# Kernel optimization log

Hardware: AMD Instinct MI355X
Metric: run time of the kernel (lower is better)

## Reference

```python
import jax, jax.numpy as jnp
import numpy as np

V, D, DFF, E, K, L = 32000, 1024, 4096, 8, 2, 2
B, S = 2, 1024


def _layer_norm(x, scale, bias, eps=1e-5):
    mu = jnp.mean(x, axis=-1, keepdims=True)
    var = jnp.var(x, axis=-1, keepdims=True)
    return (x - mu) * jax.lax.rsqrt(var + eps) * scale + bias


def setup_inputs() -> dict:
    key = jax.random.key(0)
    ks = jax.random.split(key, 16)
    s = 0.02
    return {
        "input_ids": jax.random.randint(ks[0], (B, S), 0, V, dtype=jnp.int32),
        "emb": jax.random.normal(ks[1], (V, D), jnp.float32) * s,
        "t_ln_scale": jnp.ones((L, D), jnp.float32),
        "t_ln_bias": jnp.zeros((L, D), jnp.float32),
        "t_w1": jax.random.normal(ks[2], (L, D, DFF), jnp.float32) * s,
        "t_b1": jnp.zeros((L, DFF), jnp.float32),
        "t_w2": jax.random.normal(ks[3], (L, DFF, D), jnp.float32) * s,
        "t_b2": jnp.zeros((L, D), jnp.float32),
        "Wr": jax.random.normal(ks[4], (D, E), jnp.float32) * s,
        "br": jnp.zeros((E,), jnp.float32),
        "e_w1": jax.random.normal(ks[5], (E, D, DFF), jnp.float32) * s,
        "e_b1": jnp.zeros((E, DFF), jnp.float32),
        "e_w2": jax.random.normal(ks[6], (E, DFF, D), jnp.float32) * s,
        "e_b2": jnp.zeros((E, D), jnp.float32),
        "Wl": jax.random.normal(ks[7], (D, V), jnp.float32) * s,
        "bl": jnp.zeros((V,), jnp.float32),
    }


def reference(input_ids, emb, t_ln_scale, t_ln_bias, t_w1, t_b1, t_w2, t_b2,
              Wr, br, e_w1, e_b1, e_w2, e_b2, Wl, bl):
    # token embeddings: [B,S,D]
    x = emb[input_ids]

    # temporal abstraction: L pre-LN residual MLP blocks
    for l in range(L):
        h = _layer_norm(x, t_ln_scale[l], t_ln_bias[l])
        h = jax.nn.gelu(jnp.einsum('bsd,df->bsf', h, t_w1[l]) + t_b1[l])
        x = x + jnp.einsum('bsf,fd->bsd', h, t_w2[l]) + t_b2[l]

    # router: top-k renormalized softmax over experts, scattered to [B,S,E]
    r_logits = jnp.einsum('bsd,de->bse', x, Wr) + br
    top_vals, top_idx = jax.lax.top_k(r_logits, K)
    top_w = jax.nn.softmax(top_vals, axis=-1)
    routing_weights = jnp.put_along_axis(
        jnp.zeros_like(r_logits), top_idx, top_w, axis=-1, inplace=False)

    # dense all-experts stack: [B,S,E,D]
    h = jax.nn.gelu(jnp.einsum('bsd,edf->bsef', x, e_w1) + e_b1)
    expert_out = jnp.einsum('bsef,efd->bsed', h, e_w2) + e_b2

    # sparse-weighted combine
    y = jnp.einsum('bse,bsed->bsd', routing_weights, expert_out)

    logits = jnp.einsum('bsd,dv->bsv', y, Wl) + bl
    return logits, routing_weights
```

## Files before the change

kernel.cpp:

```cpp
#include <hip/hip_runtime.h>
#include <stdint.h>

typedef __bf16 bf16;
typedef __bf16 bf16x8 __attribute__((ext_vector_type(8)));
typedef float f32x4 __attribute__((ext_vector_type(4)));

#define DEV __device__ __forceinline__

static constexpr int Dm   = 1024;
static constexpr int DFFm = 4096;
static constexpr int Tm   = 2048;
static constexpr int Vm   = 32000;

#define GLOAD_LDS16(g, l)                                                      \
  __builtin_amdgcn_global_load_lds(                                            \
      (const __attribute__((address_space(1))) unsigned int*)(g),              \
      (__attribute__((address_space(3))) unsigned int*)(l), 16, 0, 0)

DEV float gelu_tanh(float v) {
  float u = 0.7978845608028654f * (v + 0.044715f * v * v * v);
  float e = __expf(2.0f * u);
  float t = 1.0f - 2.0f / (e + 1.0f);
  return 0.5f * v * (1.0f + t);
}

enum { EPI_GELU_SPLIT = 0, EPI_RESID = 1, EPI_GELU_BF16 = 2, EPI_MOE = 3, EPI_BIAS = 4 };

struct GemmP {
  const bf16* Ah;
  const bf16* Bh;
  const float* bias;
  const float* rwp;
  const int* cnt;
  const int* idx;
  float* outF;
  bf16* outH;
  int K; int N;
  int lda; int ldb; int ldo;
  long aBS, bBS, outBS;
  int biasBS;
  int ebase;
  int kcShift; int kcK;
};

template <int EPI, bool GATHER, bool SWZ>
__launch_bounds__(256, 2)
__global__ void gemm_bt(GemmP p) {
  __shared__ bf16 lds[16384];
  bf16* ldsA = lds;
  bf16* ldsB = lds + 8192;

  const int tid  = threadIdx.x;
  const int lane = tid & 63;
  const int wid  = tid >> 6;
  const int wr   = wid >> 1;
  const int wc   = wid & 1;
  const int z    = blockIdx.z;
  const int kc   = z & ((1 << p.kcShift) - 1);
  const int ze   = z >> p.kcShift;

  int bx = blockIdx.x, by = blockIdx.y;
  if constexpr (SWZ) {
    const int gx = gridDim.x, gy = gridDim.y;
    const int nwg = gx * gy;
    const int lin = by * gx + bx;
    const int q = nwg >> 3, r = nwg & 7;
    const int xcd = lin & 7, loc = lin >> 3;
    const int nid = (xcd < r ? xcd * (q + 1) : r * (q + 1) + (xcd - r) * q) + loc;
    bx = nid / gy; by = nid % gy;
  }

  const long am0 = (long)by * 128;
  const long bn0 = (long)bx * 128;

  int cntE = 0;
  const int* il = nullptr;
  if constexpr (GATHER || EPI == EPI_MOE) {
    cntE = p.cnt[p.ebase + ze];
    if (am0 >= cntE) return;
    il = p.idx + (long)(p.ebase + ze) * 2048;
  }

  const long lda = p.lda, ldb = p.ldb;
  const long K = p.K;
  const long kco = (long)kc * p.kcK;

  const int sub = (lane & 7) ^ (lane >> 3);
  const int rIn = wid * 8 + (lane >> 3);

  const bf16 *aS[4], *bS[4];
  {
    const bf16* Bb = p.Bh + (long)ze * p.bBS + kco + bn0 * ldb;
    const bf16* Ab = p.Ah + (long)ze * p.aBS + kco + am0 * lda;
#pragma unroll
    for (int j = 0; j < 4; ++j) {
      const int row = j * 32 + rIn;
      bS[j] = Bb + (long)row * ldb + sub * 8;
      if constexpr (GATHER) {
        const int rt = (int)am0 + row;
        const long grow = il[rt < cntE ? rt : 0];
        aS[j] = p.Ah + grow * lda + kco + sub * 8;
      } else {
        aS[j] = Ab + (long)row * lda + sub * 8;
      }
    }
  }
  char* dstA[4];
#pragma unroll
  for (int j = 0; j < 4; ++j)
    dstA[j] = (char*)(void*)lds + (j * 256 + wid * 64) * 16;

  f32x4 acc[4][4] = {};

  const int r15 = lane & 15;
  const int kcs = lane >> 4;
  const int xk  = lane & 7;

  for (long k0 = 0; k0 < K; k0 += 64) {
    __syncthreads();
#pragma unroll
    for (int j = 0; j < 4; ++j) {
      GLOAD_LDS16(aS[j] + k0, dstA[j]);
      GLOAD_LDS16(bS[j] + k0, dstA[j] + 16384);
    }
    __syncthreads();
#pragma unroll
    for (int h = 0; h < 2; ++h) {
      const int q8 = ((kcs + 4 * h) ^ xk) << 3;
      bf16x8 a[4], b[4];
#pragma unroll
      for (int m = 0; m < 4; ++m)
        a[m] = *(const bf16x8*)(ldsA + (wr * 64 + m * 16 + r15) * 64 + q8);
#pragma unroll
      for (int n = 0; n < 4; ++n)
        b[n] = *(const bf16x8*)(ldsB + (wc * 64 + n * 16 + r15) * 64 + q8);
#pragma unroll
      for (int m = 0; m < 4; ++m)
#pragma unroll
        for (int n = 0; n < 4; ++n)
          acc[m][n] = __builtin_amdgcn_mfma_f32_16x16x32_bf16(a[m], b[n], acc[m][n], 0, 0, 0);
    }
  }

  const long N = p.N;

#pragma unroll
  for (int m = 0; m < 4; ++m) {
#pragma unroll
    for (int n = 0; n < 4; ++n) {
      const long col = bn0 + wc * 64 + n * 16 + (lane & 15);
      const float bv = (kc == 0) ? p.bias[(long)ze * p.biasBS + col] : 0.0f;
#pragma unroll
      for (int r = 0; r < 4; ++r) {
        const long row = am0 + wr * 64 + m * 16 + (lane >> 4) * 4 + r;
        float v = acc[m][n][r] + bv;
        if constexpr (EPI == EPI_GELU_SPLIT) {
          float g = gelu_tanh(v);
          bf16 hh = (bf16)g;
          long o = row * (long)p.ldo + col;
          p.outH[o] = hh;
          p.outH[o + N] = (bf16)(g - (float)hh);
          p.outH[o + 2 * N] = hh;
        } else if constexpr (EPI == EPI_RESID) {
          atomicAdd(p.outF + row * N + col, v);
        } else if constexpr (EPI == EPI_GELU_BF16) {
          long o = (long)ze * p.outBS + row * N + col;
          p.outH[o] = (bf16)gelu_tanh(v);
        } else if constexpr (EPI == EPI_MOE) {
          if (row < cntE) {
            const int tok = il[row];
            const float wgt = p.rwp[(long)tok * 8 + p.ebase + ze];
            atomicAdd(p.outF + (long)tok * N + col, wgt * v);
          }
        } else {
          p.outF[row * N + col] = v;
        }
      }
    }
  }
}

template <bool AUG>
__global__ void transpose_cvt(const float* __restrict__ in, bf16* __restrict__ out,
                              int R, int C, long inBS, long outBS) {
  __shared__ float tile[32][33];
  const float* inp = in + (long)blockIdx.z * inBS;
  const long c0 = (long)blockIdx.x * 32;
  const long r0 = (long)blockIdx.y * 32;
  const int tx = threadIdx.x;
  const int ty = threadIdx.y;
#pragma unroll
  for (int i = 0; i < 4; ++i) {
    int r = ty + i * 8;
    tile[r][tx] = inp[(r0 + r) * (long)C + c0 + tx];
  }
  __syncthreads();
  const long ob = (long)blockIdx.z * outBS;
  const long stride = AUG ? 3L * R : (long)R;
#pragma unroll
  for (int i = 0; i < 4; ++i) {
    int c = ty + i * 8;
    float v = tile[tx][c];
    bf16 h = (bf16)v;
    long o = ob + (c0 + c) * stride + r0 + tx;
    out[o] = h;
    if constexpr (AUG) {
      out[o + R] = h;
      out[o + 2 * R] = (bf16)(v - (float)h);
    }
  }
}

__global__ void embed_kernel(const int* __restrict__ ids, const float* __restrict__ emb,
                             float* __restrict__ x) {
  const long t = blockIdx.x;
  const int id = ids[t];
  ((float4*)(x + t * 1024))[threadIdx.x] = ((const float4*)(emb + (long)id * 1024))[threadIdx.x];
}

__global__ void ln_aug_kernel(const float* __restrict__ x, const float* __restrict__ sc,
                              const float* __restrict__ bi, bf16* __restrict__ oa) {
  const long t = blockIdx.x;
  const int tid = threadIdx.x;
  const int lane = tid & 63, wid = tid >> 6;
  float4 a = ((const float4*)(x + t * 1024))[tid];
  float s = a.x + a.y + a.z + a.w;
  float q = a.x * a.x + a.y * a.y + a.z * a.z + a.w * a.w;
#pragma unroll
  for (int off = 32; off; off >>= 1) {
    s += __shfl_down(s, off);
    q += __shfl_down(q, off);
  }
  __shared__ float sr[4], qr[4];
  if (lane == 0) { sr[wid] = s; qr[wid] = q; }
  __syncthreads();
  s = sr[0] + sr[1] + sr[2] + sr[3];
  q = qr[0] + qr[1] + qr[2] + qr[3];
  const float mu = s * (1.0f / 1024.0f);
  const float var = q * (1.0f / 1024.0f) - mu * mu;
  const float rs = rsqrtf(var + 1e-5f);
#pragma unroll
  for (int j = 0; j < 4; ++j) {
    const int d = tid * 4 + j;
    const float g = (((const float*)&a)[j] - mu) * rs * sc[d] + bi[d];
    const bf16 h = (bf16)g;
    oa[t * 3072 + d] = h;
    oa[t * 3072 + 1024 + d] = (bf16)(g - (float)h);
    oa[t * 3072 + 2048 + d] = h;
  }
}

__global__ void router_kernel(const float* __restrict__ x, const float* __restrict__ Wr,
                              const float* __restrict__ br, float* __restrict__ rwo,
                              int* __restrict__ top2) {
  const long t = blockIdx.x;
  const int lane = threadIdx.x;
  float acc[8];
#pragma unroll
  for (int e = 0; e < 8; ++e) acc[e] = 0.0f;
  const float4* xr = (const float4*)(x + t * 1024);
#pragma unroll
  for (int j = 0; j < 4; ++j) {
    const int d4 = j * 64 + lane;
    float4 xv = xr[d4];
#pragma unroll
    for (int u = 0; u < 4; ++u) {
      const float xs = ((const float*)&xv)[u];
      const float4* wp = (const float4*)(Wr + (long)(d4 * 4 + u) * 8);
      float4 w0 = wp[0], w1 = wp[1];
      acc[0] += xs * w0.x; acc[1] += xs * w0.y; acc[2] += xs * w0.z; acc[3] += xs * w0.w;
      acc[4] += xs * w1.x; acc[5] += xs * w1.y; acc[6] += xs * w1.z; acc[7] += xs * w1.w;
    }
  }
#pragma unroll
  for (int off = 32; off; off >>= 1)
#pragma unroll
    for (int e = 0; e < 8; ++e) acc[e] += __shfl_down(acc[e], off);
  if (lane == 0) {
    float v[8];
#pragma unroll
    for (int e = 0; e < 8; ++e) v[e] = acc[e] + br[e];
    int i0 = 0; float v0 = v[0];
    for (int e = 1; e < 8; ++e) if (v[e] > v0) { v0 = v[e]; i0 = e; }
    int i1 = -1; float v1 = -3.4e38f;
    for (int e = 0; e < 8; ++e) if (e != i0 && v[e] > v1) { v1 = v[e]; i1 = e; }
    float e1 = expf(v1 - v0);
    float den = 1.0f + e1;
    float w0 = 1.0f / den, w1 = e1 / den;
    float* o = rwo + t * 8;
#pragma unroll
    for (int e = 0; e < 8; ++e) o[e] = (e == i0) ? w0 : (e == i1 ? w1 : 0.0f);
    top2[t] = i0 | (i1 << 8);
  }
}

__global__ void build_lists(const int* __restrict__ top2, int* __restrict__ cnt,
                            int* __restrict__ idx) {
  const int t = blockIdx.x * 256 + threadIdx.x;
  const int rec = top2[t];
  const int e0 = rec & 255, e1 = (rec >> 8) & 255;
  int p0 = atomicAdd(&cnt[e0], 1);
  idx[e0 * 2048 + p0] = t;
  int p1 = atomicAdd(&cnt[e1], 1);
  idx[e1 * 2048 + p1] = t;
}

__global__ void cvt_bf16_kernel(const float* __restrict__ in, bf16* __restrict__ out, long n) {
  long i = ((long)blockIdx.x * blockDim.x + threadIdx.x) * 8;
  if (i >= n) return;
  float4 a = *(const float4*)(in + i);
  float4 b = *(const float4*)(in + i + 4);
  bf16x8 o;
  o[0] = (bf16)a.x; o[1] = (bf16)a.y; o[2] = (bf16)a.z; o[3] = (bf16)a.w;
  o[4] = (bf16)b.x; o[5] = (bf16)b.y; o[6] = (bf16)b.z; o[7] = (bf16)b.w;
  *(bf16x8*)(out + i) = o;
}

extern "C" void kernel_launch(void* const* d_in, const int* in_sizes, int n_in,
                              void* d_out, int out_size, void* d_ws, size_t ws_size,
                              hipStream_t stream) {
  (void)in_sizes; (void)n_in; (void)out_size; (void)ws_size;
  const int*   ids  = (const int*)d_in[0];
  const float* emb  = (const float*)d_in[1];
  const float* tlns = (const float*)d_in[2];
  const float* tlnb = (const float*)d_in[3];
  const float* tw1  = (const float*)d_in[4];
  const float* tb1  = (const float*)d_in[5];
  const float* tw2  = (const float*)d_in[6];
  const float* tb2  = (const float*)d_in[7];
  const float* Wr   = (const float*)d_in[8];
  const float* br   = (const float*)d_in[9];
  const float* ew1  = (const float*)d_in[10];
  const float* eb1  = (const float*)d_in[11];
  const float* ew2  = (const float*)d_in[12];
  const float* eb2  = (const float*)d_in[13];
  const float* Wl   = (const float*)d_in[14];
  const float* bl   = (const float*)d_in[15];

  float* logits = (float*)d_out;
  float* rwout  = (float*)d_out + (long)Tm * Vm;

  size_t off = 0;
  auto take = [&](size_t bytes) {
    void* pp = (char*)d_ws + off;
    off += (bytes + 255) & ~(size_t)255;
    return pp;
  };
  float* X    = (float*)take((size_t)Tm * Dm * 4);
  bf16*  XB   = (bf16*) take((size_t)Tm * Dm * 2);
  float* Y    = (float*)take((size_t)Tm * Dm * 4);
  bf16*  YB   = (bf16*) take((size_t)Tm * Dm * 2);
  int*   top2 = (int*)  take((size_t)Tm * 4);
  int*   cnt  = (int*)  take(8 * 4);
  int*   idxl = (int*)  take((size_t)8 * Tm * 4);
  char*  S    = (char*) take(134217728);

  bf16* A1  = (bf16*)S;
  bf16* W1A = (bf16*)(S + 12582912);
  bf16* W2A = (bf16*)(S + 12582912 + 25165824);
  bf16* HTA = (bf16*)(S + 12582912 + 2 * 25165824);
  bf16* EW1T = (bf16*)S;
  bf16* HE   = (bf16*)(S + 33554432);
  bf16* EW2T = (bf16*)(S + 100663296);
  bf16* WLT  = (bf16*)S;

  embed_kernel<<<dim3(Tm), dim3(256), 0, stream>>>(ids, emb, X);

  for (int l = 0; l < 2; ++l) {
    transpose_cvt<true><<<dim3(DFFm / 32, Dm / 32, 1), dim3(32, 8), 0, stream>>>(
        tw1 + (long)l * Dm * DFFm, W1A, Dm, DFFm, 0, 0);
    transpose_cvt<true><<<dim3(Dm / 32, DFFm / 32, 1), dim3(32, 8), 0, stream>>>(
        tw2 + (long)l * DFFm * Dm, W2A, DFFm, Dm, 0, 0);
    ln_aug_kernel<<<dim3(Tm), dim3(256), 0, stream>>>(X, tlns + l * Dm, tlnb + l * Dm, A1);

    GemmP p1{};
    p1.Ah = A1; p1.Bh = W1A;
    p1.bias = tb1 + (long)l * DFFm;
    p1.outH = HTA;
    p1.K = 3072; p1.N = DFFm; p1.lda = 3072; p1.ldb = 3072; p1.ldo = 3 * DFFm;
    gemm_bt<EPI_GELU_SPLIT, false, true>
        <<<dim3(DFFm / 128, Tm / 128, 1), dim3(256), 0, stream>>>(p1);

    GemmP p2{};
    p2.Ah = HTA; p2.Bh = W2A;
    p2.bias = tb2 + (long)l * Dm;
    p2.outF = X;
    p2.K = 1536; p2.N = Dm; p2.lda = 12288; p2.ldb = 12288;
    p2.kcShift = 3; p2.kcK = 1536;
    gemm_bt<EPI_RESID, false, true>
        <<<dim3(Dm / 128, Tm / 128, 8), dim3(256), 0, stream>>>(p2);
  }

  router_kernel<<<dim3(Tm), dim3(64), 0, stream>>>(X, Wr, br, rwout, top2);
  hipMemsetAsync(cnt, 0, 8 * 4, stream);
  build_lists<<<dim3(Tm / 256), dim3(256), 0, stream>>>(top2, cnt, idxl);
  cvt_bf16_kernel<<<dim3(Tm * Dm / (256 * 8)), dim3(256), 0, stream>>>(X, XB, (long)Tm * Dm);
  hipMemsetAsync(Y, 0, (size_t)Tm * Dm * 4, stream);

  for (int q = 0; q < 2; ++q) {
    transpose_cvt<false><<<dim3(DFFm / 32, Dm / 32, 4), dim3(32, 8), 0, stream>>>(
        ew1 + (long)q * 4 * Dm * DFFm, EW1T, Dm, DFFm, (long)Dm * DFFm, (long)DFFm * Dm);
    transpose_cvt<false><<<dim3(Dm / 32, DFFm / 32, 4), dim3(32, 8), 0, stream>>>(
        ew2 + (long)q * 4 * DFFm * Dm, EW2T, DFFm, Dm, (long)DFFm * Dm, (long)Dm * DFFm);

    GemmP pe1{};
    pe1.Ah = XB; pe1.Bh = EW1T;
    pe1.bias = eb1 + (long)q * 4 * DFFm; pe1.biasBS = DFFm;
    pe1.outH = HE; pe1.outBS = (long)Tm * DFFm;
    pe1.aBS = 0; pe1.bBS = (long)DFFm * Dm;
    pe1.cnt = cnt; pe1.idx = idxl; pe1.ebase = q * 4;
    pe1.K = Dm; pe1.N = DFFm; pe1.lda = Dm; pe1.ldb = Dm;
    gemm_bt<EPI_GELU_BF16, true, true>
        <<<dim3(DFFm / 128, Tm / 128, 4), dim3(256), 0, stream>>>(pe1);

    GemmP pe2{};
    pe2.Ah = HE; pe2.aBS = (long)Tm * DFFm;
    pe2.Bh = EW2T; pe2.bBS = (long)Dm * DFFm;
    pe2.bias = eb2 + (long)q * 4 * Dm; pe2.biasBS = Dm;
    pe2.rwp = rwout; pe2.cnt = cnt; pe2.idx = idxl; pe2.ebase = q * 4;
    pe2.outF = Y;
    pe2.K = 1024; pe2.N = Dm; pe2.lda = DFFm; pe2.ldb = DFFm;
    pe2.kcShift = 2; pe2.kcK = 1024;
    gemm_bt<EPI_MOE, false, true>
        <<<dim3(Dm / 128, Tm / 128, 16), dim3(256), 0, stream>>>(pe2);
  }

  cvt_bf16_kernel<<<dim3(Tm * Dm / (256 * 8)), dim3(256), 0, stream>>>(Y, YB, (long)Tm * Dm);
  transpose_cvt<false><<<dim3(Vm / 32, Dm / 32, 1), dim3(32, 8), 0, stream>>>(
      Wl, WLT, Dm, Vm, 0, 0);
  GemmP pl{};
  pl.Ah = YB; pl.Bh = WLT; pl.bias = bl;
  pl.outF = logits;
  pl.K = Dm; pl.N = Vm; pl.lda = Dm; pl.ldb = Dm;
  gemm_bt<EPI_BIAS, false, true>
      <<<dim3(Vm / 128, Tm / 128, 1), dim3(256), 0, stream>>>(pl);
}
```

Baseline: 1.007 ms.

## Add dedicated 256x256-tile LM-head GEMM with XCD swizzle and double buffering

Replaces the generic 128x128 gemm_bt launch for the final vocabulary projection with a new 512-thread kernel that computes 256x256 output tiles. It double-buffers K-slices into LDS via global_load_lds with an XOR swizzle, and raises wave priority around the MFMA bursts. It also remaps block IDs so neighbouring tiles land on the same XCD. The goal is more operand reuse per LDS load and better L2 locality on the largest GEMM. The trade-off is a 128KB LDS footprint that limits occupancy to about one block per CU, and the kernel assumes dimensions divisible by 256.

```diff
diff --git a/kernel.cpp b/kernel.cpp
--- a/kernel.cpp
+++ b/kernel.cpp
@@ -180,6 +180,129 @@
   }
 }
 
+template <bool SWZ>
+__launch_bounds__(512, 2)
+__global__ void gemm256_bias(const bf16* __restrict__ A, const bf16* __restrict__ B,
+                             const float* __restrict__ bias, float* __restrict__ out,
+                             int Kc, int Nc) {
+  __shared__ bf16 lds[65536];
+
+  const int tid  = threadIdx.x;
+  const int lane = tid & 63;
+  const int wid  = tid >> 6;
+  const int wr   = wid >> 2;
+  const int wc   = wid & 3;
+
+  int bx = blockIdx.x, by = blockIdx.y;
+  if constexpr (SWZ) {
+    const int gx = gridDim.x, gy = gridDim.y;
+    const int nwg = gx * gy;
+    const int lin = by * gx + bx;
+    const int q = nwg >> 3, r = nwg & 7;
+    const int xcd = lin & 7, loc = lin >> 3;
+    const int nid = (xcd < r ? xcd * (q + 1) : r * (q + 1) + (xcd - r) * q) + loc;
+    bx = nid / gy; by = nid % gy;
+  }
+  const long am0 = (long)by * 256;
+  const long bn0 = (long)bx * 256;
+  const long K = Kc;
+  const int NT = Kc >> 6;
+
+  const int sub = (lane & 7) ^ (lane >> 3);
+  const int rw  = wid * 8 + (lane >> 3);
+  const bf16 *aS[4], *bS[4];
+#pragma unroll
+  for (int j = 0; j < 4; ++j) {
+    const int row = j * 64 + rw;
+    aS[j] = A + (am0 + row) * K + sub * 8;
+    bS[j] = B + (bn0 + row) * K + sub * 8;
+  }
+
+  f32x4 acc[8][4] = {};
+  const int r15 = lane & 15;
+  const int kcs = lane >> 4;
+  const int xk  = lane & 7;
+
+  auto stage = [&](int kt, int buf) {
+    const long ko = (long)kt * 64;
+    char* base = (char*)(void*)lds + buf * 65536;
+#pragma unroll
+    for (int j = 0; j < 4; ++j) {
+      char* d = base + (j * 64 + wid * 8) * 128;
+      GLOAD_LDS16(aS[j] + ko, d);
+      GLOAD_LDS16(bS[j] + ko, d + 32768);
+    }
+  };
+
+  stage(0, 0);
+  stage(1, 1);
+
+  for (int kt = 0; kt < NT; ++kt) {
+    const int cur = kt & 1;
+    if (kt < NT - 1) asm volatile("s_waitcnt vmcnt(8)" ::: "memory");
+    else             asm volatile("s_waitcnt vmcnt(0)" ::: "memory");
+    __builtin_amdgcn_s_barrier();
+
+    const bf16* LA = lds + cur * 32768;
+    const bf16* LB = LA + 16384;
+
+    bf16x8 a0[8], b0[4];
+    {
+      const int q8 = (kcs ^ xk) << 3;
+#pragma unroll
+      for (int m = 0; m < 8; ++m)
+        a0[m] = *(const bf16x8*)(LA + (wr * 128 + m * 16 + r15) * 64 + q8);
+#pragma unroll
+      for (int n = 0; n < 4; ++n)
+        b0[n] = *(const bf16x8*)(LB + (wc * 64 + n * 16 + r15) * 64 + q8);
+    }
+    __builtin_amdgcn_s_setprio(1);
+#pragma unroll
+    for (int m = 0; m < 8; ++m)
+#pragma unroll
+      for (int n = 0; n < 4; ++n)
+        acc[m][n] = __builtin_amdgcn_mfma_f32_16x16x32_bf16(a0[m], b0[n], acc[m][n], 0, 0, 0);
+    __builtin_amdgcn_s_setprio(0);
+
+    bf16x8 a1[8], b1[4];
+    {
+      const int q8 = ((kcs + 4) ^ xk) << 3;
+#pragma unroll
+      for (int m = 0; m < 8; ++m)
+        a1[m] = *(const bf16x8*)(LA + (wr * 128 + m * 16 + r15) * 64 + q8);
+#pragma unroll
+      for (int n = 0; n < 4; ++n)
+        b1[n] = *(const bf16x8*)(LB + (wc * 64 + n * 16 + r15) * 64 + q8);
+    }
+    asm volatile("s_waitcnt lgkmcnt(0)" ::: "memory");
+    __builtin_amdgcn_s_barrier();
+    if (kt + 2 < NT) stage(kt + 2, cur);
+
+    __builtin_amdgcn_s_setprio(1);
+#pragma unroll
+    for (int m = 0; m < 8; ++m)
+#pragma unroll
+      for (int n = 0; n < 4; ++n)
+        acc[m][n] = __builtin_amdgcn_mfma_f32_16x16x32_bf16(a1[m], b1[n], acc[m][n], 0, 0, 0);
+    __builtin_amdgcn_s_setprio(0);
+  }
+
+  const long N = Nc;
+#pragma unroll
+  for (int m = 0; m < 8; ++m) {
+#pragma unroll
+    for (int n = 0; n < 4; ++n) {
+      const long col = bn0 + wc * 64 + n * 16 + r15;
+      const float bv = bias[col];
+#pragma unroll
+      for (int r = 0; r < 4; ++r) {
+        const long row = am0 + wr * 128 + m * 16 + (lane >> 4) * 4 + r;
+        out[row * N + col] = acc[m][n][r] + bv;
+      }
+    }
+  }
+}
+
 template <bool AUG>
 __global__ void transpose_cvt(const float* __restrict__ in, bf16* __restrict__ out,
                               int R, int C, long inBS, long outBS) {
@@ -428,10 +551,6 @@
   cvt_bf16_kernel<<<dim3(Tm * Dm / (256 * 8)), dim3(256), 0, stream>>>(Y, YB, (long)Tm * Dm);
   transpose_cvt<false><<<dim3(Vm / 32, Dm / 32, 1), dim3(32, 8), 0, stream>>>(
       Wl, WLT, Dm, Vm, 0, 0);
-  GemmP pl{};
-  pl.Ah = YB; pl.Bh = WLT; pl.bias = bl;
-  pl.outF = logits;
-  pl.K = Dm; pl.N = Vm; pl.lda = Dm; pl.ldb = Dm;
-  gemm_bt<EPI_BIAS, false, true>
-      <<<dim3(Vm / 128, Tm / 128, 1), dim3(256), 0, stream>>>(pl);
-}
+  gemm256_bias<true><<<dim3(Vm / 256, Tm / 256, 1), dim3(512), 0, stream>>>(
+      YB, WLT, bl, logits, Dm, Vm);
+}
```

Result: faster. 980.5 us (-2.6%).
